# Kernel optimization log

Hardware: AMD Instinct MI355X
Metric: run time of the kernel (lower is better)

The kernel has to match this reference:

```python
import jax, jax.numpy as jnp
import numpy as np

N = 50000
E = 800000
D = 128
L = 3
EPS = 1e-5


def setup_inputs() -> dict:
    key = jax.random.key(0)
    ks = jax.random.split(key, 8)
    x = jax.random.normal(ks[0], (N, D), dtype=jnp.float32)
    edge_index = jax.random.randint(ks[1], (2, E), 0, N, dtype=jnp.int64)
    s = 1.0 / np.sqrt(D)
    # stacked per-layer params (all layers are 128->128)
    Wl = jax.random.uniform(ks[2], (L, D, D), jnp.float32, -s, s)  # lin_l weight
    bl = jax.random.uniform(ks[3], (L, D), jnp.float32, -s, s)     # lin_l bias
    Wr = jax.random.uniform(ks[4], (L, D, D), jnp.float32, -s, s)  # lin_r weight (no bias)
    gamma = jnp.ones((L, D), jnp.float32)
    beta = jnp.zeros((L, D), jnp.float32)
    return {"x": x, "edge_index": edge_index, "Wl": Wl, "bl": bl,
            "Wr": Wr, "gamma": gamma, "beta": beta}


def layer_norm(h, g, b):
    mu = jnp.mean(h, axis=-1, keepdims=True)
    var = jnp.mean(jnp.square(h - mu), axis=-1, keepdims=True)
    return (h - mu) * jax.lax.rsqrt(var + EPS) * g + b


def reference(x, edge_index, Wl, bl, Wr, gamma, beta):
    src = edge_index[0]
    dst = edge_index[1]
    # in-degree counts (constant wrt features)
    cnt = jax.ops.segment_sum(jnp.ones((E,), jnp.float32), dst, num_segments=N)
    inv_cnt = (1.0 / jnp.maximum(cnt, 1.0))[:, None]  # [N,1]
    h = x
    for l in range(L):
        # mean neighbor aggregation: gather source feats, scatter-add to dst
        agg = jax.ops.segment_sum(h[src], dst, num_segments=N) * inv_cnt
        # SAGEConv: lin_l(agg) + lin_r(h)
        h2 = agg @ Wl[l].T + bl[l] + h @ Wr[l].T
        h2 = layer_norm(h2, gamma[l], beta[l])
        h = jax.nn.relu(h2)  # dropout is identity at inference
    return h
```

## Files before the change

kernel.cpp:

```cpp
#include <hip/hip_runtime.h>
#include <hip/hip_bf16.h>
#include <stdint.h>

#define NN 50000
#define EE 800000
#define DD 128
#define LL 3
#define FILL_CHUNKS 98

typedef __attribute__((ext_vector_type(8))) short short8;
typedef __attribute__((ext_vector_type(4))) float float4v;

__device__ __forceinline__ float bf2f(unsigned int u) {
  union { unsigned int i; float f; } x; x.i = u << 16; return x.f;
}
__device__ __forceinline__ unsigned short f2bf(float f) {
  union { float f; unsigned int i; } x; x.f = f;
  unsigned int r = x.i + 0x7FFFu + ((x.i >> 16) & 1u);
  return (unsigned short)(r >> 16);
}

__global__ void deg_kernel(const int* __restrict__ dst, int* __restrict__ deg, int E) {
  int e = blockIdx.x * blockDim.x + threadIdx.x;
  if (e < E) atomicAdd(&deg[__builtin_nontemporal_load(dst + e)], 1);
}

__global__ __launch_bounds__(256) void scan1_kernel(
    const int* __restrict__ deg, int* __restrict__ incl, int* __restrict__ partial, int N) {
  __shared__ int wsums[4];
  const int tid = threadIdx.x, lane = tid & 63, wid = tid >> 6;
  int i = blockIdx.x * 256 + tid;
  int v = (i < N) ? deg[i] : 0;
  int x = v;
#pragma unroll
  for (int off = 1; off < 64; off <<= 1) {
    int y = __shfl_up(x, off, 64);
    if (lane >= off) x += y;
  }
  if (lane == 63) wsums[wid] = x;
  __syncthreads();
  if (tid == 0) {
    int a0 = wsums[0], a1 = wsums[1], a2 = wsums[2];
    wsums[0] = 0; wsums[1] = a0; wsums[2] = a0 + a1; wsums[3] = a0 + a1 + a2;
  }
  __syncthreads();
  int inc = wsums[wid] + x;
  if (i < N) incl[i] = inc;
  if (tid == 255) partial[blockIdx.x] = inc;
}

__global__ __launch_bounds__(256) void scan2_kernel(int* __restrict__ partial, int P) {
  __shared__ int wsums[4];
  const int tid = threadIdx.x, lane = tid & 63, wid = tid >> 6;
  int v = (tid < P) ? partial[tid] : 0;
  int x = v;
#pragma unroll
  for (int off = 1; off < 64; off <<= 1) {
    int y = __shfl_up(x, off, 64);
    if (lane >= off) x += y;
  }
  if (lane == 63) wsums[wid] = x;
  __syncthreads();
  if (tid == 0) {
    int a0 = wsums[0], a1 = wsums[1], a2 = wsums[2];
    wsums[0] = 0; wsums[1] = a0; wsums[2] = a0 + a1; wsums[3] = a0 + a1 + a2;
  }
  __syncthreads();
  int excl = wsums[wid] + x - v;
  if (tid < P) partial[tid] = excl;
}

__global__ __launch_bounds__(256) void scan3_kernel(
    const int* __restrict__ incl, const int* __restrict__ deg, const int* __restrict__ partial,
    int* __restrict__ rowptr, int* __restrict__ cursor, int N) {
  int i = blockIdx.x * 256 + threadIdx.x;
  if (i < N) {
    int rp = incl[i] - deg[i] + partial[blockIdx.x];
    rowptr[i] = rp;
    cursor[i] = rp;
  }
  if (i == 0) rowptr[N] = EE;
}

__global__ __launch_bounds__(256) void fill_kernel(
    const int* __restrict__ src, const int* __restrict__ dst,
    int* __restrict__ cursor, int* __restrict__ col, int E) {
  const int range = blockIdx.x & 7;
  const int chunk = blockIdx.x >> 3;
  const int lo = range * (NN / 8);
  const int hi = lo + (NN / 8);
  const int per = (E + FILL_CHUNKS - 1) / FILL_CHUNKS;
  const int e0 = chunk * per;
  const int e1 = (e0 + per < E) ? (e0 + per) : E;
  for (int e = e0 + threadIdx.x; e < e1; e += 256) {
    int d = __builtin_nontemporal_load(dst + e);
    if (d >= lo && d < hi) {
      int sv = __builtin_nontemporal_load(src + e);
      int pos = atomicAdd(&cursor[d], 1);
      col[pos] = sv;
    }
  }
}

__global__ void convert_kernel(const float* __restrict__ x, unsigned short* __restrict__ hbf, int n4) {
  int i = blockIdx.x * blockDim.x + threadIdx.x;
  if (i < n4) {
    float4 v = ((const float4*)x)[i];
    ushort4 o;
    o.x = f2bf(v.x); o.y = f2bf(v.y); o.z = f2bf(v.z); o.w = f2bf(v.w);
    ((ushort4*)hbf)[i] = o;
  }
}

__global__ void repack_kernel(const float* __restrict__ Wl, const float* __restrict__ Wr,
                              unsigned short* __restrict__ out) {
  int tid = blockIdx.x * blockDim.x + threadIdx.x;
  if (tid >= LL * 8 * 8 * 64) return;
  int lane = tid & 63;
  int t = (tid >> 6) & 7;
  int ks = (tid >> 9) & 7;
  int l = tid >> 12;
  int n = t * 16 + (lane & 15);
  int kbase = ks * 32 + (lane >> 4) * 8;
  const float* Wsrc = (ks < 4) ? (Wl + ((size_t)(l * 128 + n) * 128 + kbase))
                               : (Wr + ((size_t)(l * 128 + n) * 128 + (kbase - 128)));
#pragma unroll
  for (int j = 0; j < 8; j++) out[(size_t)tid * 8 + j] = f2bf(Wsrc[j]);
}

__global__ __launch_bounds__(256) void agg_kernel(
    const unsigned short* __restrict__ hbf, const int* __restrict__ rowptr,
    const int* __restrict__ col, unsigned short* __restrict__ agg, int N) {
  int node = blockIdx.x * 4 + (threadIdx.x >> 6);
  if (node >= N) return;
  int lane = threadIdx.x & 63;
  int s = rowptr[node], e = rowptr[node + 1];
  float ax = 0.f, ay = 0.f;
  int i = s;
  for (; i + 15 < e; i += 16) {
    int idx[16];
#pragma unroll
    for (int j = 0; j < 16; j++) idx[j] = col[i + j];
    unsigned int r[16];
#pragma unroll
    for (int j = 0; j < 16; j++) r[j] = ((const unsigned int*)(hbf + (size_t)idx[j] * 128))[lane];
#pragma unroll
    for (int j = 0; j < 16; j++) {
      ax += bf2f(r[j] & 0xffffu);
      ay += bf2f(r[j] >> 16);
    }
  }
  if (i + 7 < e) {
    int idx[8];
#pragma unroll
    for (int j = 0; j < 8; j++) idx[j] = col[i + j];
    unsigned int r[8];
#pragma unroll
    for (int j = 0; j < 8; j++) r[j] = ((const unsigned int*)(hbf + (size_t)idx[j] * 128))[lane];
#pragma unroll
    for (int j = 0; j < 8; j++) {
      ax += bf2f(r[j] & 0xffffu);
      ay += bf2f(r[j] >> 16);
    }
    i += 8;
  }
  if (i + 3 < e) {
    int idx[4];
#pragma unroll
    for (int j = 0; j < 4; j++) idx[j] = col[i + j];
    unsigned int r[4];
#pragma unroll
    for (int j = 0; j < 4; j++) r[j] = ((const unsigned int*)(hbf + (size_t)idx[j] * 128))[lane];
#pragma unroll
    for (int j = 0; j < 4; j++) {
      ax += bf2f(r[j] & 0xffffu);
      ay += bf2f(r[j] >> 16);
    }
    i += 4;
  }
  for (; i < e; i++) {
    unsigned int r0 = ((const unsigned int*)(hbf + (size_t)col[i] * 128))[lane];
    ax += bf2f(r0 & 0xffffu);
    ay += bf2f(r0 >> 16);
  }
  int dg = e - s;
  float inv = 1.0f / (float)(dg > 1 ? dg : 1);
  ax *= inv; ay *= inv;
  ((unsigned int*)(agg + (size_t)node * 128))[lane] =
      ((unsigned int)f2bf(ay) << 16) | (unsigned int)f2bf(ax);
}

template <bool LAST>
__global__ __launch_bounds__(256) void gemm_ln_mfma_kernel(
    const unsigned short* __restrict__ agg, const unsigned short* __restrict__ h,
    const unsigned short* __restrict__ Bf, const float* __restrict__ bias,
    const float* __restrict__ gamma, const float* __restrict__ beta,
    unsigned short* __restrict__ out_bf, float* __restrict__ f_out, int N) {
  __shared__ unsigned short Bl[8 * 8 * 512];
  __shared__ float reds[64][16];
  __shared__ float redss[64][16];
  __shared__ float mu_s[64], rs_s[64];
  const int tid = threadIdx.x;
  {
    const uint4* srcB = (const uint4*)Bf;
    uint4* dstB = (uint4*)Bl;
#pragma unroll
    for (int i = 0; i < 16; i++) dstB[tid + i * 256] = srcB[tid + i * 256];
  }
  __syncthreads();
  const int wave = tid >> 6, lane = tid & 63;
  const int ln16 = lane & 15, quad = lane >> 4;
  const int m0 = blockIdx.x * 64 + wave * 16;
  int row_a = m0 + ln16;
  if (row_a > N - 1) row_a = N - 1;
  const size_t aoff = (size_t)row_a * 128 + quad * 8;

  float4v acc[8];
#pragma unroll
  for (int t = 0; t < 8; t++) acc[t] = (float4v)0.f;

#pragma unroll
  for (int ks = 0; ks < 8; ks++) {
    const unsigned short* ap = (ks < 4) ? (agg + aoff + ks * 32) : (h + aoff + (ks - 4) * 32);
    short8 a = *(const short8*)ap;
#pragma unroll
    for (int t = 0; t < 8; t++) {
      short8 b = *(const short8*)&Bl[(ks * 8 + t) * 512 + lane * 8];
      acc[t] = __builtin_amdgcn_mfma_f32_16x16x32_bf16(a, b, acc[t], 0, 0, 0);
    }
  }

  float bias_v[8], g_v[8], b_v[8];
#pragma unroll
  for (int t = 0; t < 8; t++) {
    int c = t * 16 + ln16;
    bias_v[t] = bias[c]; g_v[t] = gamma[c]; b_v[t] = beta[c];
  }
#pragma unroll
  for (int r = 0; r < 4; r++) {
    float s = 0.f, ss = 0.f;
#pragma unroll
    for (int t = 0; t < 8; t++) {
      float val = acc[t][r] + bias_v[t];
      s += val; ss += val * val;
    }
    int rowblk = wave * 16 + quad * 4 + r;
    reds[rowblk][ln16] = s;
    redss[rowblk][ln16] = ss;
  }
  __syncthreads();
  if (tid < 64) {
    float s = 0.f, ss = 0.f;
#pragma unroll
    for (int g = 0; g < 16; g++) { s += reds[tid][g]; ss += redss[tid][g]; }
    float mu = s * (1.0f / 128.0f);
    float var = ss * (1.0f / 128.0f) - mu * mu;
    if (var < 0.f) var = 0.f;
    mu_s[tid] = mu;
    rs_s[tid] = rsqrtf(var + 1e-5f);
  }
  __syncthreads();
#pragma unroll
  for (int r = 0; r < 4; r++) {
    int row = m0 + quad * 4 + r;
    int rowblk = wave * 16 + quad * 4 + r;
    if (row < N) {
      float mu = mu_s[rowblk], rs = rs_s[rowblk];
#pragma unroll
      for (int t = 0; t < 8; t++) {
        float val = acc[t][r] + bias_v[t];
        float y = (val - mu) * rs * g_v[t] + b_v[t];
        y = y > 0.f ? y : 0.f;
        int cidx = t * 16 + ln16;
        if (LAST) {
          f_out[(size_t)row * 128 + cidx] = y;
        } else {
          out_bf[(size_t)row * 128 + cidx] = f2bf(y);
        }
      }
    }
  }
}

extern "C" void kernel_launch(void* const* d_in, const int* in_sizes, int n_in,
                              void* d_out, int out_size, void* d_ws, size_t ws_size,
                              hipStream_t stream) {
  const float* x = (const float*)d_in[0];
  const int* edge = (const int*)d_in[1];
  const float* Wl = (const float*)d_in[2];
  const float* bl = (const float*)d_in[3];
  const float* Wr = (const float*)d_in[4];
  const float* gamma = (const float*)d_in[5];
  const float* beta = (const float*)d_in[6];
  float* out = (float*)d_out;

  const int* srcv = edge;
  const int* dstv = edge + EE;

  char* p = (char*)d_ws;
  auto alloc = [&](size_t bytes) {
    char* r = p;
    p += (bytes + 255) & ~(size_t)255;
    return r;
  };
  const size_t bplane = (size_t)NN * 128 * 2;
  unsigned short* xB = (unsigned short*)alloc(bplane);
  unsigned short* h1B = (unsigned short*)alloc(bplane);
  unsigned short* h2B = (unsigned short*)alloc(bplane);
  unsigned short* agB = (unsigned short*)alloc(bplane);
  unsigned short* BfB = (unsigned short*)alloc((size_t)LL * 32768 * 2);
  int* deg = (int*)alloc((size_t)NN * 4);
  int* incl = (int*)alloc((size_t)NN * 4);
  int* cursor = (int*)alloc((size_t)NN * 4);
  int* rowptr = (int*)alloc((size_t)(NN + 1) * 4);
  int* colarr = (int*)alloc((size_t)EE * 4);
  int* partial = (int*)alloc((size_t)256 * 4);
  if ((size_t)(p - (char*)d_ws) > ws_size) return;

  const int SCAN_BLOCKS = (NN + 255) / 256;

  hipMemsetAsync(deg, 0, (size_t)NN * 4, stream);
  deg_kernel<<<(EE + 255) / 256, 256, 0, stream>>>(dstv, deg, EE);
  scan1_kernel<<<SCAN_BLOCKS, 256, 0, stream>>>(deg, incl, partial, NN);
  scan2_kernel<<<1, 256, 0, stream>>>(partial, SCAN_BLOCKS);
  scan3_kernel<<<SCAN_BLOCKS, 256, 0, stream>>>(incl, deg, partial, rowptr, cursor, NN);
  fill_kernel<<<8 * FILL_CHUNKS, 256, 0, stream>>>(srcv, dstv, cursor, colarr, EE);
  convert_kernel<<<(NN * 128 / 4 + 255) / 256, 256, 0, stream>>>(x, xB, NN * 128 / 4);
  repack_kernel<<<(LL * 4096 + 255) / 256, 256, 0, stream>>>(Wl, Wr, BfB);

  const int gemm_grid = (NN + 63) / 64;
  const int agg_grid = (NN + 3) / 4;

  agg_kernel<<<agg_grid, 256, 0, stream>>>(xB, rowptr, colarr, agB, NN);
  gemm_ln_mfma_kernel<false><<<gemm_grid, 256, 0, stream>>>(
      agB, xB, BfB, bl, gamma, beta, h1B, nullptr, NN);

  agg_kernel<<<agg_grid, 256, 0, stream>>>(h1B, rowptr, colarr, agB, NN);
  gemm_ln_mfma_kernel<false><<<gemm_grid, 256, 0, stream>>>(
      agB, h1B, BfB + 32768, bl + 128, gamma + 128, beta + 128, h2B, nullptr, NN);

  agg_kernel<<<agg_grid, 256, 0, stream>>>(h2B, rowptr, colarr, agB, NN);
  gemm_ln_mfma_kernel<true><<<gemm_grid, 256, 0, stream>>>(
      agB, h2B, BfB + 2 * 32768, bl + 256, gamma + 256, beta + 256, nullptr, out, NN);
}
```

Baseline: 316.0 us.

## Build CSR via two-pass bucketed counting sort with LDS-local fill

Replaces the per-edge global atomic CSR fill with two stages. First, edges are binned into 512-node destination buckets using shared-memory histograms and one global atomic per bucket per tile, and written as packed (local dst, src) pairs. Then one block per bucket scatters those pairs into an LDS column buffer using LDS atomics and writes it out contiguously. This removes global atomic contention and scattered writes. It adds an extra pass over the edges and packs src into 16 bits, which cannot hold node ids up to 50000 once they exceed 65535… they don't here, so it is fine but fragile.

Measured after the change: 345.1 us. 1.09x slower.

```diff
diff --git a/kernel.cpp b/kernel.cpp
--- a/kernel.cpp
+++ b/kernel.cpp
@@ -6,7 +6,8 @@
 #define EE 800000
 #define DD 128
 #define LL 3
-#define FILL_CHUNKS 98
+#define NBUCK 98
+#define SEG_CAP 10240
 
 typedef __attribute__((ext_vector_type(8))) short short8;
 typedef __attribute__((ext_vector_type(4))) float float4v;
@@ -72,32 +73,74 @@
 
 __global__ __launch_bounds__(256) void scan3_kernel(
     const int* __restrict__ incl, const int* __restrict__ deg, const int* __restrict__ partial,
-    int* __restrict__ rowptr, int* __restrict__ cursor, int N) {
+    int* __restrict__ rowptr, int* __restrict__ bcursor, int N) {
   int i = blockIdx.x * 256 + threadIdx.x;
   if (i < N) {
     int rp = incl[i] - deg[i] + partial[blockIdx.x];
     rowptr[i] = rp;
-    cursor[i] = rp;
+    if ((i & 511) == 0) bcursor[i >> 9] = rp;
   }
   if (i == 0) rowptr[N] = EE;
 }
 
-__global__ __launch_bounds__(256) void fill_kernel(
+__global__ __launch_bounds__(256) void bucket_kernel(
     const int* __restrict__ src, const int* __restrict__ dst,
-    int* __restrict__ cursor, int* __restrict__ col, int E) {
-  const int range = blockIdx.x & 7;
-  const int chunk = blockIdx.x >> 3;
-  const int lo = range * (NN / 8);
-  const int hi = lo + (NN / 8);
-  const int per = (E + FILL_CHUNKS - 1) / FILL_CHUNKS;
-  const int e0 = chunk * per;
+    int* __restrict__ bcursor, unsigned int* __restrict__ pairbuf, int E) {
+  __shared__ int hist[NBUCK];
+  __shared__ int gbase[NBUCK];
+  const int tid = threadIdx.x;
+  const int per = (E + gridDim.x - 1) / gridDim.x;
+  const int e0 = blockIdx.x * per;
   const int e1 = (e0 + per < E) ? (e0 + per) : E;
-  for (int e = e0 + threadIdx.x; e < e1; e += 256) {
-    int d = __builtin_nontemporal_load(dst + e);
-    if (d >= lo && d < hi) {
-      int sv = __builtin_nontemporal_load(src + e);
-      int pos = atomicAdd(&cursor[d], 1);
-      col[pos] = sv;
+  for (int base = e0; base < e1; base += 256) {
+    if (tid < NBUCK) hist[tid] = 0;
+    __syncthreads();
+    int e = base + tid;
+    bool valid = e < e1;
+    int d = 0, s = 0, b = 0, rank = 0;
+    if (valid) {
+      d = __builtin_nontemporal_load(dst + e);
+      s = __builtin_nontemporal_load(src + e);
+      b = d >> 9;
+      rank = atomicAdd(&hist[b], 1);
+    }
+    __syncthreads();
+    if (tid < NBUCK && hist[tid] > 0) gbase[tid] = atomicAdd(&bcursor[tid], hist[tid]);
+    __syncthreads();
+    if (valid)
+      pairbuf[gbase[b] + rank] = ((unsigned int)(d & 511) << 16) | (unsigned int)s;
+    __syncthreads();
+  }
+}
+
+__global__ __launch_bounds__(256) void csrfill_kernel(
+    const unsigned int* __restrict__ pairbuf, const int* __restrict__ rowptr,
+    int* __restrict__ col) {
+  __shared__ int off[513];
+  __shared__ int lcur[512];
+  __shared__ int lcol[SEG_CAP];
+  const int tid = threadIdx.x;
+  const int lo = blockIdx.x * 512;
+  const int nmax = (NN - lo < 512) ? (NN - lo) : 512;
+  for (int i = tid; i <= nmax; i += 256) off[i] = rowptr[lo + i];
+  for (int i = tid; i < nmax; i += 256) lcur[i] = 0;
+  __syncthreads();
+  const int base = off[0], end = off[nmax], seg = end - base;
+  if (seg <= SEG_CAP) {
+    for (int e = base + tid; e < end; e += 256) {
+      unsigned int pk = pairbuf[e];
+      int d = pk >> 16, s = pk & 0xFFFFu;
+      int pos = atomicAdd(&lcur[d], 1);
+      lcol[off[d] - base + pos] = s;
+    }
+    __syncthreads();
+    for (int i = tid; i < seg; i += 256) col[base + i] = lcol[i];
+  } else {
+    for (int e = base + tid; e < end; e += 256) {
+      unsigned int pk = pairbuf[e];
+      int d = pk >> 16, s = pk & 0xFFFFu;
+      int pos = atomicAdd(&lcur[d], 1);
+      col[off[d] + pos] = s;
     }
   }
 }
@@ -311,10 +354,11 @@
   unsigned short* BfB = (unsigned short*)alloc((size_t)LL * 32768 * 2);
   int* deg = (int*)alloc((size_t)NN * 4);
   int* incl = (int*)alloc((size_t)NN * 4);
-  int* cursor = (int*)alloc((size_t)NN * 4);
   int* rowptr = (int*)alloc((size_t)(NN + 1) * 4);
   int* colarr = (int*)alloc((size_t)EE * 4);
+  unsigned int* pairbuf = (unsigned int*)alloc((size_t)EE * 4);
   int* partial = (int*)alloc((size_t)256 * 4);
+  int* bcursor = (int*)alloc((size_t)256 * 4);
   if ((size_t)(p - (char*)d_ws) > ws_size) return;
 
   const int SCAN_BLOCKS = (NN + 255) / 256;
@@ -323,8 +367,9 @@
   deg_kernel<<<(EE + 255) / 256, 256, 0, stream>>>(dstv, deg, EE);
   scan1_kernel<<<SCAN_BLOCKS, 256, 0, stream>>>(deg, incl, partial, NN);
   scan2_kernel<<<1, 256, 0, stream>>>(partial, SCAN_BLOCKS);
-  scan3_kernel<<<SCAN_BLOCKS, 256, 0, stream>>>(incl, deg, partial, rowptr, cursor, NN);
-  fill_kernel<<<8 * FILL_CHUNKS, 256, 0, stream>>>(srcv, dstv, cursor, colarr, EE);
+  scan3_kernel<<<SCAN_BLOCKS, 256, 0, stream>>>(incl, deg, partial, rowptr, bcursor, NN);
+  bucket_kernel<<<256, 256, 0, stream>>>(srcv, dstv, bcursor, pairbuf, EE);
+  csrfill_kernel<<<NBUCK, 256, 0, stream>>>(pairbuf, rowptr, colarr);
   convert_kernel<<<(NN * 128 / 4 + 255) / 256, 256, 0, stream>>>(x, xB, NN * 128 / 4);
   repack_kernel<<<(LL * 4096 + 255) / 256, 256, 0, stream>>>(Wl, Wr, BfB);
 
```
